# Kernel optimization log

Hardware: AMD Instinct MI355X
Metric: run time of the kernel (lower is better)

## Reference

```python
import jax, jax.numpy as jnp
import numpy as np

TOP_K = 8
NUM_EXPERTS = 128
HIDDEN = 2048
TOKENS = 16384
NORM_TOPK_PROB = True


def setup_inputs() -> dict:
    key = jax.random.key(0)
    k1, k2 = jax.random.split(key)
    hidden_states = jax.random.normal(k1, (TOKENS, HIDDEN), dtype=jnp.float32)
    # gate weight [num_experts, hidden] (nn.Linear layout)
    weight = jax.random.normal(k2, (NUM_EXPERTS, HIDDEN), dtype=jnp.float32) * 0.02
    return {"hidden_states": hidden_states, "weight": weight}


def reference(hidden_states, weight):
    x = hidden_states.reshape(-1, HIDDEN)
    # router_logits: [tokens, num_experts]
    router_logits = jnp.einsum("td,ed->te", x, weight)
    router_probs = jax.nn.softmax(router_logits.astype(jnp.float32), axis=-1)
    top_vals, top_idx = jax.lax.top_k(router_probs, TOP_K)
    if NORM_TOPK_PROB:
        top_vals = top_vals / jnp.sum(top_vals, axis=-1, keepdims=True)
    top_vals = top_vals.astype(hidden_states.dtype)
    return router_logits, top_vals, top_idx
```

## Files before the change

kernel.cpp:

```cpp
#include <hip/hip_runtime.h>
#include <float.h>
#include <math.h>

#define TOKENS 16384
#define HIDDEN 2048
#define NEXP 128
#define TOPK 8
#define NCAND 12
#define DELTA 5e-4f

#define BM 32
#define BK 64
#define KITERS (HIDDEN / BK)

typedef float f32x16 __attribute__((ext_vector_type(16)));
typedef short bf16x8 __attribute__((ext_vector_type(8)));

__device__ __forceinline__ unsigned pack_hi(float a, float b) {
    return (__float_as_uint(a) >> 16) | (__float_as_uint(b) & 0xFFFF0000u);
}
__device__ __forceinline__ float resid(float a) {
    return a - __uint_as_float(__float_as_uint(a) & 0xFFFF0000u);
}

__device__ __forceinline__ void load_lds_16B(const void* g, void* l) {
    __builtin_amdgcn_global_load_lds(
        (const __attribute__((address_space(1))) unsigned int*)g,
        (__attribute__((address_space(3))) unsigned int*)l, 16, 0, 0);
}

__global__ __launch_bounds__(256) void presplit_w(const float* __restrict__ W,
                                                  unsigned short* __restrict__ Ws) {
    const int c = blockIdx.x * 256 + threadIdx.x;
    const int lane = c & 63;
    const int q = c >> 6;
    const int hl = q & 1;
    const int nt = (q >> 1) & 3;
    const int k16 = q >> 3;
    const int e = nt * 32 + (lane & 31);
    const int k0 = k16 * 16 + (lane >> 5) * 8;
    const float* wp = W + (size_t)e * HIDDEN + k0;
    float4 a = *(const float4*)wp;
    float4 b = *(const float4*)(wp + 4);
    if (hl) {
        a.x = resid(a.x); a.y = resid(a.y); a.z = resid(a.z); a.w = resid(a.w);
        b.x = resid(b.x); b.y = resid(b.y); b.z = resid(b.z); b.w = resid(b.w);
    }
    uint4 o;
    o.x = pack_hi(a.x, a.y); o.y = pack_hi(a.z, a.w);
    o.z = pack_hi(b.x, b.y); o.w = pack_hi(b.z, b.w);
    *(uint4*)(Ws + (size_t)c * 8) = o;
}

__global__ __launch_bounds__(256) void router_gemm(const float* __restrict__ X,
                                                   const unsigned short* __restrict__ Ws,
                                                   float* __restrict__ logits) {
    __shared__ unsigned short sA[8 * 512];
    __shared__ unsigned short sB[32 * 512];
    const int tid = threadIdx.x;
    const int lane = tid & 63;
    const int wid = tid >> 6;
    const int t0 = blockIdx.x * BM;

    const int arow = tid >> 3, aq = tid & 7;
    const int offH = ((aq >> 1) * 2 + 0) * 512 + ((aq & 1) * 32 + arow) * 8;
    const int offL = offH + 512;
    const float* Xp = X + (size_t)(t0 + arow) * HIDDEN + aq * 8;

    f32x16 acc;
#pragma unroll
    for (int r = 0; r < 16; ++r) acc[r] = 0.f;

    float4 xa = *(const float4*)(Xp);
    float4 xb = *(const float4*)(Xp + 4);

#pragma unroll 1
    for (int kt = 0; kt < KITERS; ++kt) {
        __syncthreads();
        {
            const unsigned short* src = Ws + ((size_t)kt * 32 + wid * 8) * 512 + lane * 8;
            unsigned short* dst = &sB[(wid * 8) * 512];
#pragma unroll
            for (int i = 0; i < 8; ++i)
                load_lds_16B(src + i * 512, dst + i * 512);
        }
        {
            uint4 v;
            v.x = pack_hi(xa.x, xa.y); v.y = pack_hi(xa.z, xa.w);
            v.z = pack_hi(xb.x, xb.y); v.w = pack_hi(xb.z, xb.w);
            *(uint4*)&sA[offH] = v;
            v.x = pack_hi(resid(xa.x), resid(xa.y));
            v.y = pack_hi(resid(xa.z), resid(xa.w));
            v.z = pack_hi(resid(xb.x), resid(xb.y));
            v.w = pack_hi(resid(xb.z), resid(xb.w));
            *(uint4*)&sA[offL] = v;
        }
        __syncthreads();

        if (kt + 1 < KITERS) {
            const float* xp = Xp + (kt + 1) * BK;
            xa = *(const float4*)(xp);
            xb = *(const float4*)(xp + 4);
        }

#pragma unroll
        for (int s = 0; s < 4; ++s) {
            const bf16x8 ah = *(const bf16x8*)&sA[(s * 2 + 0) * 512 + lane * 8];
            const bf16x8 al = *(const bf16x8*)&sA[(s * 2 + 1) * 512 + lane * 8];
            const int bb = (s * 8 + wid * 2) * 512 + lane * 8;
            const bf16x8 bh = *(const bf16x8*)&sB[bb];
            const bf16x8 bl = *(const bf16x8*)&sB[bb + 512];
            acc = __builtin_amdgcn_mfma_f32_32x32x16_bf16(ah, bh, acc, 0, 0, 0);
            acc = __builtin_amdgcn_mfma_f32_32x32x16_bf16(ah, bl, acc, 0, 0, 0);
            acc = __builtin_amdgcn_mfma_f32_32x32x16_bf16(al, bh, acc, 0, 0, 0);
        }
    }

    const int e = wid * 32 + (lane & 31);
    const int rbase = 4 * (lane >> 5);
#pragma unroll
    for (int reg = 0; reg < 16; ++reg) {
        const int row = (reg & 3) + 8 * (reg >> 2) + rbase;
        logits[(size_t)(t0 + row) * NEXP + e] = acc[reg];
    }
}

__global__ __launch_bounds__(256) void router_topk(const float* __restrict__ logits,
                                                   const float* __restrict__ X,
                                                   const float* __restrict__ W,
                                                   float* __restrict__ top_vals,
                                                   float* __restrict__ top_idx) {
    const int lane = threadIdx.x & 63;
    const int t = blockIdx.x * 4 + (threadIdx.x >> 6);
    const float* lrow = logits + (size_t)t * NEXP;
    const float l0 = lrow[lane];
    const float l1 = lrow[lane + 64];
    bool r0 = false, r1 = false;
    float vals[NCAND]; int idxs[NCAND];

#pragma unroll
    for (int it = 0; it < TOPK + 1; ++it) {
        const float c0 = r0 ? -FLT_MAX : l0;
        const float c1 = r1 ? -FLT_MAX : l1;
        float v; int id;
        if (c1 > c0) { v = c1; id = lane + 64; }
        else         { v = c0; id = lane; }
#pragma unroll
        for (int off = 1; off < 64; off <<= 1) {
            const float ov = __shfl_xor(v, off);
            const int   oi = __shfl_xor(id, off);
            if (ov > v || (ov == v && oi < id)) { v = ov; id = oi; }
        }
        vals[it] = v; idxs[it] = id;
        if (id == lane) r0 = true;
        else if (id == lane + 64) r1 = true;
    }

    float ming = FLT_MAX;
#pragma unroll
    for (int i = 0; i < TOPK; ++i) ming = fminf(ming, vals[i] - vals[i + 1]);

    if (ming >= DELTA) {
        if (lane == 0) {
            const float m = vals[0];
            float ex[TOPK], s = 0.f;
#pragma unroll
            for (int i = 0; i < TOPK; ++i) { ex[i] = expf(vals[i] - m); s += ex[i]; }
            const float inv = 1.f / s;
#pragma unroll
            for (int i = 0; i < TOPK; ++i) {
                top_vals[(size_t)t * TOPK + i] = ex[i] * inv;
                top_idx[(size_t)t * TOPK + i] = (float)idxs[i];
            }
        }
        return;
    }

#pragma unroll
    for (int it = TOPK + 1; it < NCAND; ++it) {
        const float c0 = r0 ? -FLT_MAX : l0;
        const float c1 = r1 ? -FLT_MAX : l1;
        float v; int id;
        if (c1 > c0) { v = c1; id = lane + 64; }
        else         { v = c0; id = lane; }
#pragma unroll
        for (int off = 1; off < 64; off <<= 1) {
            const float ov = __shfl_xor(v, off);
            const int   oi = __shfl_xor(id, off);
            if (ov > v || (ov == v && oi < id)) { v = ov; id = oi; }
        }
        vals[it] = v; idxs[it] = id;
        if (id == lane) r0 = true;
        else if (id == lane + 64) r1 = true;
    }

    const float* xr = X + (size_t)t * HIDDEN;
    double xd[32];
#pragma unroll
    for (int j = 0; j < 8; ++j) {
        const float4 v = *(const float4*)(xr + j * 256 + lane * 4);
        xd[j * 4 + 0] = (double)v.x; xd[j * 4 + 1] = (double)v.y;
        xd[j * 4 + 2] = (double)v.z; xd[j * 4 + 3] = (double)v.w;
    }
    double acc[NCAND];
#pragma unroll
    for (int c = 0; c < NCAND; ++c) {
        const float* wr = W + (size_t)idxs[c] * HIDDEN;
        double a0 = 0.0, a1 = 0.0;
#pragma unroll
        for (int j = 0; j < 8; ++j) {
            const float4 w = *(const float4*)(wr + j * 256 + lane * 4);
            a0 = fma((double)w.x, xd[j * 4 + 0], a0);
            a1 = fma((double)w.y, xd[j * 4 + 1], a1);
            a0 = fma((double)w.z, xd[j * 4 + 2], a0);
            a1 = fma((double)w.w, xd[j * 4 + 3], a1);
        }
        acc[c] = a0 + a1;
    }
#pragma unroll
    for (int c = 0; c < NCAND; ++c)
#pragma unroll
        for (int off = 1; off < 64; off <<= 1)
            acc[c] += __shfl_xor(acc[c], off);

    int rank[NCAND];
#pragma unroll
    for (int c = 0; c < NCAND; ++c) {
        int r = 0;
#pragma unroll
        for (int m = 0; m < NCAND; ++m)
            if (acc[m] > acc[c] || (acc[m] == acc[c] && idxs[m] < idxs[c])) ++r;
        rank[c] = r;
    }
    double vmax = acc[0];
#pragma unroll
    for (int c = 0; c < NCAND; ++c) if (rank[c] == 0) vmax = acc[c];
    float ex[NCAND], s = 0.f;
#pragma unroll
    for (int c = 0; c < NCAND; ++c) {
        ex[c] = (rank[c] < TOPK) ? expf((float)(acc[c] - vmax)) : 0.f;
        s += ex[c];
    }
    const float inv = 1.f / s;
    if (lane == 0) {
#pragma unroll
        for (int c = 0; c < NCAND; ++c)
            if (rank[c] < TOPK) {
                top_vals[(size_t)t * TOPK + rank[c]] = ex[c] * inv;
                top_idx[(size_t)t * TOPK + rank[c]] = (float)idxs[c];
            }
    }
}

extern "C" void kernel_launch(void* const* d_in, const int* in_sizes, int n_in,
                              void* d_out, int out_size, void* d_ws, size_t ws_size,
                              hipStream_t stream) {
    const float* X = (const float*)d_in[0];
    const float* W = (const float*)d_in[1];
    float* logits = (float*)d_out;
    float* tvals  = logits + (size_t)TOKENS * NEXP;
    float* tidx   = tvals + (size_t)TOKENS * TOPK;

    unsigned short* Wsplit = (unsigned short*)d_ws;

    presplit_w<<<256, 256, 0, stream>>>(W, Wsplit);
    router_gemm<<<TOKENS / BM, 256, 0, stream>>>(X, Wsplit, logits);
    router_topk<<<TOKENS / 4, 256, 0, stream>>>(logits, X, W, tvals, tidx);
}
```

Before: 293.7 us.

## Split GEMM over expert halves with split-K waves and two-tokens-per-wave top-k

The router GEMM now splits the 128 experts across two blocks per 32-token tile, and each of the four waves handles a separate K slice with BK doubled. The waves convert X to bf16 hi/lo in registers instead of staging it through LDS, then combine their partial sums through an LDS reduction at the end. Top-k now processes two tokens per wave using 32-lane shuffles, and the exact fp64 fallback is moved into a helper called only for flagged tokens. The aim is more blocks in flight, no A-tile LDS traffic, and fewer shuffle steps, at the cost of reading X twice and an extra cross-wave reduction.

```diff
diff --git a/kernel.cpp b/kernel.cpp
--- a/kernel.cpp
+++ b/kernel.cpp
@@ -10,7 +10,7 @@
 #define DELTA 5e-4f
 
 #define BM 32
-#define BK 64
+#define BK 128
 #define KITERS (HIDDEN / BK)
 
 typedef float f32x16 __attribute__((ext_vector_type(16)));
@@ -21,6 +21,18 @@
 }
 __device__ __forceinline__ float resid(float a) {
     return a - __uint_as_float(__float_as_uint(a) & 0xFFFF0000u);
+}
+__device__ __forceinline__ bf16x8 to_hi(float4 a, float4 b) {
+    union { unsigned u[4]; bf16x8 v; } r;
+    r.u[0] = pack_hi(a.x, a.y); r.u[1] = pack_hi(a.z, a.w);
+    r.u[2] = pack_hi(b.x, b.y); r.u[3] = pack_hi(b.z, b.w);
+    return r.v;
+}
+__device__ __forceinline__ bf16x8 to_lo(float4 a, float4 b) {
+    union { unsigned u[4]; bf16x8 v; } r;
+    r.u[0] = pack_hi(resid(a.x), resid(a.y)); r.u[1] = pack_hi(resid(a.z), resid(a.w));
+    r.u[2] = pack_hi(resid(b.x), resid(b.y)); r.u[3] = pack_hi(resid(b.z), resid(b.w));
+    return r.v;
 }
 
 __device__ __forceinline__ void load_lds_16B(const void* g, void* l) {
@@ -35,93 +47,211 @@
     const int lane = c & 63;
     const int q = c >> 6;
     const int hl = q & 1;
-    const int nt = (q >> 1) & 3;
-    const int k16 = q >> 3;
-    const int e = nt * 32 + (lane & 31);
-    const int k0 = k16 * 16 + (lane >> 5) * 8;
+    const int nt = (q >> 1) & 1;
+    const int s = (q >> 2) & 7;
+    const int egrp = (q >> 5) & 1;
+    const int kt = q >> 6;
+    const int e = egrp * 64 + nt * 32 + (lane & 31);
+    const int k0 = kt * 128 + s * 16 + (lane >> 5) * 8;
     const float* wp = W + (size_t)e * HIDDEN + k0;
     float4 a = *(const float4*)wp;
     float4 b = *(const float4*)(wp + 4);
+    uint4 o;
     if (hl) {
-        a.x = resid(a.x); a.y = resid(a.y); a.z = resid(a.z); a.w = resid(a.w);
-        b.x = resid(b.x); b.y = resid(b.y); b.z = resid(b.z); b.w = resid(b.w);
-    }
-    uint4 o;
-    o.x = pack_hi(a.x, a.y); o.y = pack_hi(a.z, a.w);
-    o.z = pack_hi(b.x, b.y); o.w = pack_hi(b.z, b.w);
+        o.x = pack_hi(resid(a.x), resid(a.y)); o.y = pack_hi(resid(a.z), resid(a.w));
+        o.z = pack_hi(resid(b.x), resid(b.y)); o.w = pack_hi(resid(b.z), resid(b.w));
+    } else {
+        o.x = pack_hi(a.x, a.y); o.y = pack_hi(a.z, a.w);
+        o.z = pack_hi(b.x, b.y); o.w = pack_hi(b.z, b.w);
+    }
     *(uint4*)(Ws + (size_t)c * 8) = o;
 }
 
-__global__ __launch_bounds__(256) void router_gemm(const float* __restrict__ X,
-                                                   const unsigned short* __restrict__ Ws,
-                                                   float* __restrict__ logits) {
-    __shared__ unsigned short sA[8 * 512];
+__global__ __launch_bounds__(256, 4) void router_gemm(const float* __restrict__ X,
+                                                      const unsigned short* __restrict__ Ws,
+                                                      float* __restrict__ logits) {
     __shared__ unsigned short sB[32 * 512];
     const int tid = threadIdx.x;
     const int lane = tid & 63;
-    const int wid = tid >> 6;
-    const int t0 = blockIdx.x * BM;
-
-    const int arow = tid >> 3, aq = tid & 7;
-    const int offH = ((aq >> 1) * 2 + 0) * 512 + ((aq & 1) * 32 + arow) * 8;
-    const int offL = offH + 512;
-    const float* Xp = X + (size_t)(t0 + arow) * HIDDEN + aq * 8;
-
-    f32x16 acc;
-#pragma unroll
-    for (int r = 0; r < 16; ++r) acc[r] = 0.f;
-
-    float4 xa = *(const float4*)(Xp);
-    float4 xb = *(const float4*)(Xp + 4);
+    const int w = tid >> 6;
+    const int t0 = (blockIdx.x >> 1) * BM;
+    const int egrp = blockIdx.x & 1;
+
+    const float* Xp = X + (size_t)(t0 + (lane & 31)) * HIDDEN + w * 32 + ((lane >> 5) * 8);
+
+    f32x16 acc[2];
+#pragma unroll
+    for (int nt = 0; nt < 2; ++nt)
+#pragma unroll
+        for (int r = 0; r < 16; ++r) acc[nt][r] = 0.f;
+
+    float4 xv[4];
+    xv[0] = *(const float4*)(Xp);
+    xv[1] = *(const float4*)(Xp + 4);
+    xv[2] = *(const float4*)(Xp + 16);
+    xv[3] = *(const float4*)(Xp + 20);
 
 #pragma unroll 1
     for (int kt = 0; kt < KITERS; ++kt) {
         __syncthreads();
         {
-            const unsigned short* src = Ws + ((size_t)kt * 32 + wid * 8) * 512 + lane * 8;
-            unsigned short* dst = &sB[(wid * 8) * 512];
+            const unsigned short* src =
+                Ws + ((size_t)((kt * 2 + egrp) * 32 + w * 8)) * 512 + lane * 8;
+            unsigned short* dst = &sB[(w * 8) * 512];
 #pragma unroll
             for (int i = 0; i < 8; ++i)
                 load_lds_16B(src + i * 512, dst + i * 512);
         }
-        {
-            uint4 v;
-            v.x = pack_hi(xa.x, xa.y); v.y = pack_hi(xa.z, xa.w);
-            v.z = pack_hi(xb.x, xb.y); v.w = pack_hi(xb.z, xb.w);
-            *(uint4*)&sA[offH] = v;
-            v.x = pack_hi(resid(xa.x), resid(xa.y));
-            v.y = pack_hi(resid(xa.z), resid(xa.w));
-            v.z = pack_hi(resid(xb.x), resid(xb.y));
-            v.w = pack_hi(resid(xb.z), resid(xb.w));
-            *(uint4*)&sA[offL] = v;
-        }
         __syncthreads();
 
+        float4 xn[4];
         if (kt + 1 < KITERS) {
             const float* xp = Xp + (kt + 1) * BK;
-            xa = *(const float4*)(xp);
-            xb = *(const float4*)(xp + 4);
-        }
-
-#pragma unroll
-        for (int s = 0; s < 4; ++s) {
-            const bf16x8 ah = *(const bf16x8*)&sA[(s * 2 + 0) * 512 + lane * 8];
-            const bf16x8 al = *(const bf16x8*)&sA[(s * 2 + 1) * 512 + lane * 8];
-            const int bb = (s * 8 + wid * 2) * 512 + lane * 8;
-            const bf16x8 bh = *(const bf16x8*)&sB[bb];
-            const bf16x8 bl = *(const bf16x8*)&sB[bb + 512];
-            acc = __builtin_amdgcn_mfma_f32_32x32x16_bf16(ah, bh, acc, 0, 0, 0);
-            acc = __builtin_amdgcn_mfma_f32_32x32x16_bf16(ah, bl, acc, 0, 0, 0);
-            acc = __builtin_amdgcn_mfma_f32_32x32x16_bf16(al, bh, acc, 0, 0, 0);
-        }
-    }
-
-    const int e = wid * 32 + (lane & 31);
-    const int rbase = 4 * (lane >> 5);
-#pragma unroll
-    for (int reg = 0; reg < 16; ++reg) {
-        const int row = (reg & 3) + 8 * (reg >> 2) + rbase;
-        logits[(size_t)(t0 + row) * NEXP + e] = acc[reg];
+            xn[0] = *(const float4*)(xp);
+            xn[1] = *(const float4*)(xp + 4);
+            xn[2] = *(const float4*)(xp + 16);
+            xn[3] = *(const float4*)(xp + 20);
+        }
+
+#pragma unroll
+        for (int h = 0; h < 2; ++h) {
+            const bf16x8 ah = to_hi(xv[h * 2], xv[h * 2 + 1]);
+            const bf16x8 al = to_lo(xv[h * 2], xv[h * 2 + 1]);
+#pragma unroll
+            for (int nt = 0; nt < 2; ++nt) {
+                const int bb = ((w * 2 + h) * 4 + nt * 2) * 512 + lane * 8;
+                const bf16x8 bh = *(const bf16x8*)&sB[bb];
+                const bf16x8 bl = *(const bf16x8*)&sB[bb + 512];
+                acc[nt] = __builtin_amdgcn_mfma_f32_32x32x16_bf16(ah, bh, acc[nt], 0, 0, 0);
+                acc[nt] = __builtin_amdgcn_mfma_f32_32x32x16_bf16(ah, bl, acc[nt], 0, 0, 0);
+                acc[nt] = __builtin_amdgcn_mfma_f32_32x32x16_bf16(al, bh, acc[nt], 0, 0, 0);
+            }
+        }
+#pragma unroll
+        for (int i = 0; i < 4; ++i) xv[i] = xn[i];
+    }
+
+    __syncthreads();
+    float* red = (float*)sB;
+    if (w > 0) {
+#pragma unroll
+        for (int nt = 0; nt < 2; ++nt)
+#pragma unroll
+            for (int i = 0; i < 4; ++i) {
+                float4 v = {acc[nt][i * 4 + 0], acc[nt][i * 4 + 1],
+                            acc[nt][i * 4 + 2], acc[nt][i * 4 + 3]};
+                *(float4*)&red[(((w - 1) * 8 + nt * 4 + i) * 256) + lane * 4] = v;
+            }
+    }
+    __syncthreads();
+    if (w == 0) {
+#pragma unroll
+        for (int src = 0; src < 3; ++src)
+#pragma unroll
+            for (int nt = 0; nt < 2; ++nt)
+#pragma unroll
+                for (int i = 0; i < 4; ++i) {
+                    const float4 v = *(const float4*)&red[((src * 8 + nt * 4 + i) * 256) + lane * 4];
+                    acc[nt][i * 4 + 0] += v.x; acc[nt][i * 4 + 1] += v.y;
+                    acc[nt][i * 4 + 2] += v.z; acc[nt][i * 4 + 3] += v.w;
+                }
+        const int col = lane & 31;
+        const int rbase = 4 * (lane >> 5);
+#pragma unroll
+        for (int nt = 0; nt < 2; ++nt) {
+            const int e = egrp * 64 + nt * 32 + col;
+#pragma unroll
+            for (int reg = 0; reg < 16; ++reg) {
+                const int row = (reg & 3) + 8 * (reg >> 2) + rbase;
+                logits[(size_t)(t0 + row) * NEXP + e] = acc[nt][reg];
+            }
+        }
+    }
+}
+
+__device__ void slow_token(const float* __restrict__ lrow,
+                           const float* __restrict__ X,
+                           const float* __restrict__ W,
+                           float* __restrict__ top_vals,
+                           float* __restrict__ top_idx,
+                           int t, int lane) {
+    const float l0 = lrow[lane];
+    const float l1 = lrow[lane + 64];
+    bool r0 = false, r1 = false;
+    float vals[NCAND]; int idxs[NCAND];
+#pragma unroll
+    for (int it = 0; it < NCAND; ++it) {
+        const float c0 = r0 ? -FLT_MAX : l0;
+        const float c1 = r1 ? -FLT_MAX : l1;
+        float v; int id;
+        if (c1 > c0) { v = c1; id = lane + 64; }
+        else         { v = c0; id = lane; }
+#pragma unroll
+        for (int off = 1; off < 64; off <<= 1) {
+            const float ov = __shfl_xor(v, off);
+            const int   oi = __shfl_xor(id, off);
+            if (ov > v || (ov == v && oi < id)) { v = ov; id = oi; }
+        }
+        vals[it] = v; idxs[it] = id;
+        if (id == lane) r0 = true;
+        else if (id == lane + 64) r1 = true;
+    }
+
+    const float* xr = X + (size_t)t * HIDDEN;
+    double xd[32];
+#pragma unroll
+    for (int j = 0; j < 8; ++j) {
+        const float4 v = *(const float4*)(xr + j * 256 + lane * 4);
+        xd[j * 4 + 0] = (double)v.x; xd[j * 4 + 1] = (double)v.y;
+        xd[j * 4 + 2] = (double)v.z; xd[j * 4 + 3] = (double)v.w;
+    }
+    double acc[NCAND];
+#pragma unroll
+    for (int c = 0; c < NCAND; ++c) {
+        const float* wr = W + (size_t)idxs[c] * HIDDEN;
+        double a0 = 0.0, a1 = 0.0;
+#pragma unroll
+        for (int j = 0; j < 8; ++j) {
+            const float4 wv = *(const float4*)(wr + j * 256 + lane * 4);
+            a0 = fma((double)wv.x, xd[j * 4 + 0], a0);
+            a1 = fma((double)wv.y, xd[j * 4 + 1], a1);
+            a0 = fma((double)wv.z, xd[j * 4 + 2], a0);
+            a1 = fma((double)wv.w, xd[j * 4 + 3], a1);
+        }
+        acc[c] = a0 + a1;
+    }
+#pragma unroll
+    for (int c = 0; c < NCAND; ++c)
+#pragma unroll
+        for (int off = 1; off < 64; off <<= 1)
+            acc[c] += __shfl_xor(acc[c], off);
+
+    int rank[NCAND];
+#pragma unroll
+    for (int c = 0; c < NCAND; ++c) {
+        int r = 0;
+#pragma unroll
+        for (int m = 0; m < NCAND; ++m)
+            if (acc[m] > acc[c] || (acc[m] == acc[c] && idxs[m] < idxs[c])) ++r;
+        rank[c] = r;
+    }
+    double vmax = acc[0];
+#pragma unroll
+    for (int c = 0; c < NCAND; ++c) if (rank[c] == 0) vmax = acc[c];
+    float e[NCAND], s = 0.f;
+#pragma unroll
+    for (int c = 0; c < NCAND; ++c) {
+        e[c] = (rank[c] < TOPK) ? expf((float)(acc[c] - vmax)) : 0.f;
+        s += e[c];
+    }
+    const float inv = 1.f / s;
+    if (lane == 0) {
+#pragma unroll
+        for (int c = 0; c < NCAND; ++c)
+            if (rank[c] < TOPK) {
+                top_vals[(size_t)t * TOPK + rank[c]] = e[c] * inv;
+                top_idx[(size_t)t * TOPK + rank[c]] = (float)idxs[c];
+            }
     }
 }
 
@@ -131,125 +261,65 @@
                                                    float* __restrict__ top_vals,
                                                    float* __restrict__ top_idx) {
     const int lane = threadIdx.x & 63;
-    const int t = blockIdx.x * 4 + (threadIdx.x >> 6);
+    const int h = lane >> 5;
+    const int li = lane & 31;
+    const int tbase = blockIdx.x * 8 + (threadIdx.x >> 6) * 2;
+    const int t = tbase + h;
     const float* lrow = logits + (size_t)t * NEXP;
-    const float l0 = lrow[lane];
-    const float l1 = lrow[lane + 64];
-    bool r0 = false, r1 = false;
-    float vals[NCAND]; int idxs[NCAND];
-
+
+    float v0 = lrow[li];
+    float v1 = lrow[li + 32];
+    float v2 = lrow[li + 64];
+    float v3 = lrow[li + 96];
+    bool rm0 = false, rm1 = false, rm2 = false, rm3 = false;
+
+    float vals[TOPK + 1]; int idxs[TOPK + 1];
 #pragma unroll
     for (int it = 0; it < TOPK + 1; ++it) {
-        const float c0 = r0 ? -FLT_MAX : l0;
-        const float c1 = r1 ? -FLT_MAX : l1;
-        float v; int id;
-        if (c1 > c0) { v = c1; id = lane + 64; }
-        else         { v = c0; id = lane; }
-#pragma unroll
-        for (int off = 1; off < 64; off <<= 1) {
-            const float ov = __shfl_xor(v, off);
+        float bv = rm0 ? -FLT_MAX : v0; int bs = 0;
+        const float c1 = rm1 ? -FLT_MAX : v1;
+        const float c2 = rm2 ? -FLT_MAX : v2;
+        const float c3 = rm3 ? -FLT_MAX : v3;
+        if (c1 > bv) { bv = c1; bs = 1; }
+        if (c2 > bv) { bv = c2; bs = 2; }
+        if (c3 > bv) { bv = c3; bs = 3; }
+        int id = bs * 32 + li;
+#pragma unroll
+        for (int off = 1; off < 32; off <<= 1) {
+            const float ov = __shfl_xor(bv, off);
             const int   oi = __shfl_xor(id, off);
-            if (ov > v || (ov == v && oi < id)) { v = ov; id = oi; }
-        }
-        vals[it] = v; idxs[it] = id;
-        if (id == lane) r0 = true;
-        else if (id == lane + 64) r1 = true;
+            if (ov > bv || (ov == bv && oi < id)) { bv = ov; id = oi; }
+        }
+        vals[it] = bv; idxs[it] = id;
+        if ((id & 31) == li) {
+            const int s = id >> 5;
+            rm0 |= (s == 0); rm1 |= (s == 1); rm2 |= (s == 2); rm3 |= (s == 3);
+        }
     }
 
     float ming = FLT_MAX;
 #pragma unroll
     for (int i = 0; i < TOPK; ++i) ming = fminf(ming, vals[i] - vals[i + 1]);
-
-    if (ming >= DELTA) {
-        if (lane == 0) {
-            const float m = vals[0];
-            float ex[TOPK], s = 0.f;
-#pragma unroll
-            for (int i = 0; i < TOPK; ++i) { ex[i] = expf(vals[i] - m); s += ex[i]; }
-            const float inv = 1.f / s;
-#pragma unroll
-            for (int i = 0; i < TOPK; ++i) {
-                top_vals[(size_t)t * TOPK + i] = ex[i] * inv;
-                top_idx[(size_t)t * TOPK + i] = (float)idxs[i];
-            }
-        }
-        return;
-    }
-
-#pragma unroll
-    for (int it = TOPK + 1; it < NCAND; ++it) {
-        const float c0 = r0 ? -FLT_MAX : l0;
-        const float c1 = r1 ? -FLT_MAX : l1;
-        float v; int id;
-        if (c1 > c0) { v = c1; id = lane + 64; }
-        else         { v = c0; id = lane; }
-#pragma unroll
-        for (int off = 1; off < 64; off <<= 1) {
-            const float ov = __shfl_xor(v, off);
-            const int   oi = __shfl_xor(id, off);
-            if (ov > v || (ov == v && oi < id)) { v = ov; id = oi; }
-        }
-        vals[it] = v; idxs[it] = id;
-        if (id == lane) r0 = true;
-        else if (id == lane + 64) r1 = true;
-    }
-
-    const float* xr = X + (size_t)t * HIDDEN;
-    double xd[32];
-#pragma unroll
-    for (int j = 0; j < 8; ++j) {
-        const float4 v = *(const float4*)(xr + j * 256 + lane * 4);
-        xd[j * 4 + 0] = (double)v.x; xd[j * 4 + 1] = (double)v.y;
-        xd[j * 4 + 2] = (double)v.z; xd[j * 4 + 3] = (double)v.w;
-    }
-    double acc[NCAND];
-#pragma unroll
-    for (int c = 0; c < NCAND; ++c) {
-        const float* wr = W + (size_t)idxs[c] * HIDDEN;
-        double a0 = 0.0, a1 = 0.0;
-#pragma unroll
-        for (int j = 0; j < 8; ++j) {
-            const float4 w = *(const float4*)(wr + j * 256 + lane * 4);
-            a0 = fma((double)w.x, xd[j * 4 + 0], a0);
-            a1 = fma((double)w.y, xd[j * 4 + 1], a1);
-            a0 = fma((double)w.z, xd[j * 4 + 2], a0);
-            a1 = fma((double)w.w, xd[j * 4 + 3], a1);
-        }
-        acc[c] = a0 + a1;
-    }
-#pragma unroll
-    for (int c = 0; c < NCAND; ++c)
-#pragma unroll
-        for (int off = 1; off < 64; off <<= 1)
-            acc[c] += __shfl_xor(acc[c], off);
-
-    int rank[NCAND];
-#pragma unroll
-    for (int c = 0; c < NCAND; ++c) {
-        int r = 0;
-#pragma unroll
-        for (int m = 0; m < NCAND; ++m)
-            if (acc[m] > acc[c] || (acc[m] == acc[c] && idxs[m] < idxs[c])) ++r;
-        rank[c] = r;
-    }
-    double vmax = acc[0];
-#pragma unroll
-    for (int c = 0; c < NCAND; ++c) if (rank[c] == 0) vmax = acc[c];
-    float ex[NCAND], s = 0.f;
-#pragma unroll
-    for (int c = 0; c < NCAND; ++c) {
-        ex[c] = (rank[c] < TOPK) ? expf((float)(acc[c] - vmax)) : 0.f;
-        s += ex[c];
-    }
-    const float inv = 1.f / s;
-    if (lane == 0) {
-#pragma unroll
-        for (int c = 0; c < NCAND; ++c)
-            if (rank[c] < TOPK) {
-                top_vals[(size_t)t * TOPK + rank[c]] = ex[c] * inv;
-                top_idx[(size_t)t * TOPK + rank[c]] = (float)idxs[c];
-            }
-    }
+    const bool flag = (ming < DELTA);
+
+    if (!flag && li == 0) {
+        const float m = vals[0];
+        float ex[TOPK], s = 0.f;
+#pragma unroll
+        for (int i = 0; i < TOPK; ++i) { ex[i] = expf(vals[i] - m); s += ex[i]; }
+        const float inv = 1.f / s;
+#pragma unroll
+        for (int i = 0; i < TOPK; ++i) {
+            top_vals[(size_t)t * TOPK + i] = ex[i] * inv;
+            top_idx[(size_t)t * TOPK + i] = (float)idxs[i];
+        }
+    }
+
+    const unsigned long long bal = __ballot(flag);
+    if (bal & 1ull)
+        slow_token(logits + (size_t)tbase * NEXP, X, W, top_vals, top_idx, tbase, lane);
+    if (bal & (1ull << 32))
+        slow_token(logits + (size_t)(tbase + 1) * NEXP, X, W, top_vals, top_idx, tbase + 1, lane);
 }
 
 extern "C" void kernel_launch(void* const* d_in, const int* in_sizes, int n_in,
@@ -264,6 +334,6 @@
     unsigned short* Wsplit = (unsigned short*)d_ws;
 
     presplit_w<<<256, 256, 0, stream>>>(W, Wsplit);
-    router_gemm<<<TOKENS / BM, 256, 0, stream>>>(X, Wsplit, logits);
-    router_topk<<<TOKENS / 4, 256, 0, stream>>>(logits, X, W, tvals, tidx);
-}
+    router_gemm<<<(TOKENS / BM) * 2, 256, 0, stream>>>(X, Wsplit, logits);
+    router_topk<<<TOKENS / 8, 256, 0, stream>>>(logits, X, W, tvals, tidx);
+}
```

After: 317.9 us. +8.3%, slower.
